# Performance work log

Hardware: AMD Instinct MI355X
Metric: run time of the kernel (lower is better)

The kernel has to match this reference:

```python
import jax, jax.numpy as jnp
import numpy as np

T, B, V, E, H = 256, 64, 10000, 400, 1152


def _n(k, shape, scale=0.05):
    return jax.random.normal(k, shape, jnp.float32) * scale


def setup_inputs() -> dict:
    key = jax.random.key(0)
    ks = jax.random.split(key, 32)
    inp = {}
    inp["x"] = jax.random.randint(ks[0], (T, B), 0, V)
    inp["h0"] = _n(ks[1], (B, H)); inp["h1"] = _n(ks[2], (B, H)); inp["h2"] = _n(ks[3], (B, E))
    inp["c0"] = _n(ks[4], (B, H)); inp["c1"] = _n(ks[5], (B, H)); inp["c2"] = _n(ks[6], (B, E))
    inp["emb"] = _n(ks[7], (V, E), 0.1)
    # layer i: (input_dim, output_dim): (E,H), (H,H), (H,E)
    sizes = [(E, H), (H, H), (H, E)]
    j = 8
    for i, (din, dout) in enumerate(sizes):
        inp[f"W_ih{i}"] = _n(ks[j], (4 * dout, din)); j += 1
        inp[f"W_hh{i}"] = _n(ks[j], (4 * dout, dout)); j += 1
        inp[f"b_ih{i}"] = _n(ks[j], (4 * dout,)); j += 1
        inp[f"b_hh{i}"] = _n(ks[j], (4 * dout,)); j += 1
    inp["dec_W"] = _n(ks[j], (V, E)); j += 1
    inp["dec_b"] = jnp.zeros((V,), jnp.float32)
    return inp


def lstm_cell(x, h, c, Wih, Whh, bih, bhh):
    # PyTorch LSTMCell: gates = x@Wih^T + bih + h@Whh^T + bhh, order i,f,g,o
    g = x @ Wih.T + h @ Whh.T + bih + bhh
    i, f, gg, o = jnp.split(g, 4, axis=-1)
    c2 = jax.nn.sigmoid(f) * c + jax.nn.sigmoid(i) * jnp.tanh(gg)
    h2 = jax.nn.sigmoid(o) * jnp.tanh(c2)
    return h2, c2


def reference(x, h0, h1, h2, c0, c1, c2, emb,
              W_ih0, W_hh0, b_ih0, b_hh0,
              W_ih1, W_hh1, b_ih1, b_hh1,
              W_ih2, W_hh2, b_ih2, b_hh2,
              dec_W, dec_b):
    xe = emb[x]  # [T, B, E]

    def step(carry, xt):
        a0, a1, a2, s0, s1, s2 = carry
        a0, s0 = lstm_cell(xt, a0, s0, W_ih0, W_hh0, b_ih0, b_hh0)
        a1, s1 = lstm_cell(a0, a1, s1, W_ih1, W_hh1, b_ih1, b_hh1)
        a2, s2 = lstm_cell(a1, a2, s2, W_ih2, W_hh2, b_ih2, b_hh2)
        return (a0, a1, a2, s0, s1, s2), a2

    _, out = jax.lax.scan(step, (h0, h1, h2, c0, c1, c2), xe)  # out: [T, B, E]
    decoded = out @ dec_W.T + dec_b  # [T, B, V]
    return decoded
```

## Files before the change

kernel.cpp:

```cpp
#include <hip/hip_runtime.h>
#include <hip/hip_bf16.h>

typedef __hip_bfloat16 bf16;
typedef __attribute__((ext_vector_type(8))) short short8;
typedef __attribute__((ext_vector_type(4))) float f32x4;

#define T_ 256
#define B_ 64
#define V_ 10000
#define E_ 400
#define H_ 1152
#define KU 2304
#define XW 416
#define KD 416
#define XET (XW*B_)
#define NBLK 169

#define MFMA16 __builtin_amdgcn_mfma_f32_16x16x32_bf16
#define ATL(p) __hip_atomic_load((p), __ATOMIC_RELAXED, __HIP_MEMORY_SCOPE_AGENT)
#define ATS(p, v) __hip_atomic_store((p), (v), __ATOMIC_RELAXED, __HIP_MEMORY_SCOPE_AGENT)
#define PIN(x) asm volatile("" : "+v"(x))


__global__ __launch_bounds__(256) void prep_wint(
    const float* __restrict__ s1, int w1,
    const float* __restrict__ s2, int off2, int w2, int Hl,
    bf16* __restrict__ dst, long total)
{
    long i = (long)blockIdx.x * 256 + threadIdx.x;
    if (i >= total) return;
    int r = (int)(i / KU), k = (int)(i % KU);
    int hcol = r >> 2, gate = r & 3;
    long srow = (long)gate * Hl + hcol;
    float v = 0.f;
    if (k < w1) v = s1[srow * w1 + k];
    else if (k >= off2 && k < off2 + w2) v = s2[srow * w2 + (k - off2)];
    dst[i] = __float2bfloat16(v);
}

__global__ __launch_bounds__(256) void prep_wcat(
    const float* __restrict__ s1, int w1,
    bf16* __restrict__ dst, int Ktot, long total)
{
    long i = (long)blockIdx.x * 256 + threadIdx.x;
    if (i >= total) return;
    int k = (int)(i % Ktot);
    long n = i / Ktot;
    dst[i] = __float2bfloat16(k < w1 ? s1[n * w1 + k] : 0.f);
}

__global__ __launch_bounds__(256) void bias_int(
    const float* __restrict__ a, const float* __restrict__ b,
    int Hl, float* __restrict__ d, int n)
{
    int r = blockIdx.x * 256 + threadIdx.x;
    if (r >= n) return;
    int hcol = r >> 2, gate = r & 3;
    d[r] = a[gate * Hl + hcol] + b[gate * Hl + hcol];
}

__global__ __launch_bounds__(256) void gather_xef(
    const int* __restrict__ x, const float* __restrict__ emb,
    bf16* __restrict__ XEf)
{
    long i = (long)blockIdx.x * 256 + threadIdx.x;
    if (i >= (long)T_ * B_ * XW) return;
    int k = (int)(i % XW);
    int b = (int)((i / XW) % B_);
    int t = (int)(i / ((long)XW * B_));
    float v = (k < E_) ? emb[(long)x[t * B_ + b] * E_ + k] : 0.f;
    XEf[(long)t * XET + (((k >> 3) * 64 + b) << 3) + (k & 7)] = __float2bfloat16(v);
}

__global__ __launch_bounds__(256) void copy_hf(
    const float* __restrict__ src, bf16* __restrict__ dst, int cols, int total)
{
    int i = blockIdx.x * 256 + threadIdx.x;
    if (i >= total) return;
    int k = i % cols, b = i / cols;
    dst[(((k >> 3) * 64 + b) << 3) + (k & 7)] = __float2bfloat16(src[(long)b * cols + k]);
}

__global__ __launch_bounds__(256) void copy_f32(
    const float* __restrict__ src, float* __restrict__ dst, int n)
{
    int i = blockIdx.x * 256 + threadIdx.x;
    if (i < n) dst[i] = src[i];
}

__device__ __forceinline__ void grid_bar(int* flags, int* gen, int phase) {
    asm volatile("s_waitcnt vmcnt(0)" ::: "memory");
    __syncthreads();
    if (blockIdx.x == 0) {
        if (threadIdx.x < 64) {
            const int ln = threadIdx.x;
            if (ln == 0) ATS(&flags[0], phase);
            for (;;) {
                int f0 = (ln       < NBLK) ? ATL(&flags[ln])       : phase;
                int f1 = (ln + 64  < NBLK) ? ATL(&flags[ln + 64])  : phase;
                int f2 = (ln + 128 < NBLK) ? ATL(&flags[ln + 128]) : phase;
                if (__all(f0 >= phase && f1 >= phase && f2 >= phase)) break;
                __builtin_amdgcn_s_sleep(1);
            }
            if (ln == 0) {
                ATS(gen, phase);
                __builtin_amdgcn_fence(__ATOMIC_ACQUIRE, "agent");
            }
        }
    } else {
        if (threadIdx.x == 0) {
            ATS(&flags[blockIdx.x], phase);
            while (ATL(gen) < phase)
                __builtin_amdgcn_s_sleep(1);
            __builtin_amdgcn_fence(__ATOMIC_ACQUIRE, "agent");
        }
    }
    __syncthreads();
    asm volatile("" ::: "memory");
}

struct Frag4 { short8 f0, f1, f2, f3; };

__global__ __launch_bounds__(512, 2) void awd_persistent(
    const bf16* __restrict__ XEf,
    const bf16* __restrict__ W0, const bf16* __restrict__ W1, const bf16* __restrict__ W2,
    const float* __restrict__ b0, const float* __restrict__ b1, const float* __restrict__ b2,
    bf16* H0f0, bf16* H0f1, bf16* H1f0, bf16* H1f1, bf16* H2f0, bf16* H2f1,
    float* c0, float* c1, float* c2, bf16* OUTB,
    int* flags, int* gen)
{
    __shared__ float gsm[4][64][65];
    const int bid = blockIdx.x;
    const int tid = threadIdx.x;
    const int lane = tid & 63;
    const int w8 = tid >> 6;
    const int lh = lane >> 4, l15 = lane & 15;
    const int boff8 = (lh * 64 + l15) * 8;

    int layer, grp;
    if (bid < 72)       { layer = 1; grp = bid; }
    else if (bid < 144) { layer = 0; grp = bid - 72; }
    else                { layer = 2; grp = bid - 144; }

    const bf16* Wp  = (layer == 0) ? W0 : (layer == 1) ? W1 : W2;
    const float* bias = (layer == 0) ? b0 : (layer == 1) ? b1 : b2;
    const float* cbuf = (layer == 0) ? c0 : (layer == 1) ? c1 : c2;
    const int Hl  = (layer == 2) ? 400 : 1152;
    const int bkt = (layer == 0) ? 13 : 36;
    const int nkt = (layer == 1) ? 72 : 49;
    const int KT  = (layer == 1) ? 9  : 7;
    const int kbase = w8 * KT;

    short8 wreg[9][4];
    #pragma unroll
    for (int u = 0; u < 9; ++u)
        if (u < KT) {
            #pragma unroll
            for (int rt = 0; rt < 4; ++rt) {
                int row = grp * 64 + rt * 16 + l15;
                int k   = (kbase + u) * 32 + lh * 8;
                wreg[u][rt] = *(const short8*)(Wp + (long)row * KU + k);
                PIN(wreg[u][rt]);
            }
        }

    float myb[2][4];
    #pragma unroll
    for (int e = 0; e < 2; ++e)
        #pragma unroll
        for (int g = 0; g < 4; ++g)
            myb[e][g] = bias[grp * 64 + (w8 + e * 8) * 4 + g];

    float creg[2];
    #pragma unroll
    for (int e = 0; e < 2; ++e)
        creg[e] = cbuf[(long)lane * Hl + grp * 16 + w8 + e * 8];

    for (int s = -1; s <= 256; ++s) {
        bool active = (layer == 0) ? (s <= 254)
                    : (layer == 1) ? (s >= 0 && s <= 255)
                                   : (s >= 1);
        if (active) {
            const int p = s & 1, q = p ^ 1;
            const bf16 *A1, *A2; bf16* hfW; bf16* ob = nullptr;
            if (layer == 0) {
                A1 = XEf + (long)(s + 1) * XET;
                A2 = p ? H0f1 : H0f0;
                hfW = q ? H0f1 : H0f0;
            } else if (layer == 1) {
                A1 = p ? H0f1 : H0f0;
                A2 = q ? H1f1 : H1f0;
                hfW = p ? H1f1 : H1f0;
            } else {
                A1 = q ? H1f1 : H1f0;
                A2 = p ? H2f1 : H2f0;
                hfW = q ? H2f1 : H2f0;
                ob = OUTB + (long)(s - 1) * B_ * XW;
            }

            auto loadf = [&](int u) -> Frag4 {
                const int ktg = kbase + u;
                const bf16* src; int ktL;
                if (ktg < bkt)      { src = A1; ktL = ktg; }
                else if (ktg < nkt) { src = A2; ktL = ktg - bkt; }
                else                { src = A1; ktL = 0; }
                const bf16* pB = src + ktL * 2048 + boff8;
                Frag4 r;
                r.f0 = *(const short8*)(pB);
                r.f1 = *(const short8*)(pB + 128);
                r.f2 = *(const short8*)(pB + 256);
                r.f3 = *(const short8*)(pB + 384);
                return r;
            };

            f32x4 acc[4][4];
            #pragma unroll
            for (int rt = 0; rt < 4; ++rt)
                #pragma unroll
                for (int m = 0; m < 4; ++m)
                    acc[rt][m] = (f32x4){0.f, 0.f, 0.f, 0.f};

            auto domfma = [&](int u, const Frag4& f) {
                #pragma unroll
                for (int rt = 0; rt < 4; ++rt) {
                    acc[rt][0] = MFMA16(wreg[u][rt], f.f0, acc[rt][0], 0, 0, 0);
                    acc[rt][1] = MFMA16(wreg[u][rt], f.f1, acc[rt][1], 0, 0, 0);
                    acc[rt][2] = MFMA16(wreg[u][rt], f.f2, acc[rt][2], 0, 0, 0);
                    acc[rt][3] = MFMA16(wreg[u][rt], f.f3, acc[rt][3], 0, 0, 0);
                }
            };

            #pragma unroll
            for (int u = 0; u < 9; ++u)
                if (u < KT) {
                    Frag4 f = loadf(u);
                    domfma(u, f);
                }

            __syncthreads();
            if (w8 >= 4) {
                #pragma unroll
                for (int rt = 0; rt < 4; ++rt)
                    #pragma unroll
                    for (int m = 0; m < 4; ++m)
                        #pragma unroll
                        for (int r = 0; r < 4; ++r)
                            gsm[w8 - 4][rt * 16 + lh * 4 + r][m * 16 + l15] = acc[rt][m][r];
            }
            __syncthreads();
            if (w8 < 4) {
                #pragma unroll
                for (int rt = 0; rt < 4; ++rt)
                    #pragma unroll
                    for (int m = 0; m < 4; ++m)
                        #pragma unroll
                        for (int r = 0; r < 4; ++r)
                            gsm[w8][rt * 16 + lh * 4 + r][m * 16 + l15] += acc[rt][m][r];
            }
            __syncthreads();

            #pragma unroll
            for (int e = 0; e < 2; ++e) {
                int b = lane;
                int cl = w8 + e * 8;
                float gv[4];
                #pragma unroll
                for (int g = 0; g < 4; ++g)
                    gv[g] = gsm[0][cl * 4 + g][b] + gsm[1][cl * 4 + g][b]
                          + gsm[2][cl * 4 + g][b] + gsm[3][cl * 4 + g][b] + myb[e][g];
                int colG = grp * 16 + cl;
                float c_old = creg[e];
                float i_s = 1.f / (1.f + expf(-gv[0]));
                float f_s = 1.f / (1.f + expf(-gv[1]));
                float o_s = 1.f / (1.f + expf(-gv[3]));
                float c_new = f_s * c_old + i_s * tanhf(gv[2]);
                float hval = o_s * tanhf(c_new);
                creg[e] = c_new;
                bf16 hb = __float2bfloat16(hval);
                unsigned short hbits;
                __builtin_memcpy(&hbits, &hb, 2);
                ATS((unsigned short*)&hfW[(((colG >> 3) * 64 + b) << 3) + (colG & 7)], hbits);
                if (layer == 2) ob[(long)b * XW + colG] = hb;
            }
        }
        grid_bar(flags, gen, s + 2);
    }
}

__global__ __launch_bounds__(256) void decoder(
    const bf16* __restrict__ A, const bf16* __restrict__ W,
    const float* __restrict__ bias, float* __restrict__ out)
{
    const int tid = threadIdx.x;
    const int lane = tid & 63;
    const int w = tid >> 6;
    const int n0 = blockIdx.x * 64;
    const int m0 = blockIdx.y * 64 + w * 16;
    const int c16 = lane & 15;
    const int kg = lane >> 4;

    f32x4 acc[4];
    for (int i = 0; i < 4; ++i) acc[i] = (f32x4){0.f, 0.f, 0.f, 0.f};

    const bf16* arow = A + (long)(m0 + c16) * KD + kg * 8;
    #pragma unroll
    for (int kt = 0; kt < 13; ++kt) {
        short8 af = *(const short8*)(arow + kt * 32);
        #pragma unroll
        for (int ns = 0; ns < 4; ++ns) {
            int n = n0 + ns * 16 + c16;
            if (n > V_ - 1) n = V_ - 1;
            short8 bfr = *(const short8*)(W + (long)n * KD + kt * 32 + kg * 8);
            acc[ns] = MFMA16(af, bfr, acc[ns], 0, 0, 0);
        }
    }

    #pragma unroll
    for (int ns = 0; ns < 4; ++ns) {
        int col = n0 + ns * 16 + c16;
        if (col < V_) {
            float bv = bias[col];
            #pragma unroll
            for (int r = 0; r < 4; ++r) {
                int row = m0 + kg * 4 + r;
                out[(size_t)row * V_ + col] = acc[ns][r] + bv;
            }
        }
    }
}


extern "C" void kernel_launch(void* const* d_in, const int* in_sizes, int n_in,
                              void* d_out, int out_size, void* d_ws, size_t ws_size,
                              hipStream_t stream)
{
    const int*   x    = (const int*)d_in[0];
    const float* h0   = (const float*)d_in[1];
    const float* h1   = (const float*)d_in[2];
    const float* h2   = (const float*)d_in[3];
    const float* c0   = (const float*)d_in[4];
    const float* c1   = (const float*)d_in[5];
    const float* c2   = (const float*)d_in[6];
    const float* emb  = (const float*)d_in[7];
    const float* Wih0 = (const float*)d_in[8];
    const float* Whh0 = (const float*)d_in[9];
    const float* bih0 = (const float*)d_in[10];
    const float* bhh0 = (const float*)d_in[11];
    const float* Wih1 = (const float*)d_in[12];
    const float* Whh1 = (const float*)d_in[13];
    const float* bih1 = (const float*)d_in[14];
    const float* bhh1 = (const float*)d_in[15];
    const float* Wih2 = (const float*)d_in[16];
    const float* Whh2 = (const float*)d_in[17];
    const float* bih2 = (const float*)d_in[18];
    const float* bhh2 = (const float*)d_in[19];
    const float* decW = (const float*)d_in[20];
    const float* decb = (const float*)d_in[21];

    char* wsb = (char*)d_ws;
    size_t off = 0;
    auto alloc = [&](size_t bytes) -> void* {
        void* ptr = wsb + off;
        off = (off + bytes + 255) & ~(size_t)255;
        return ptr;
    };

    bf16* W0i = (bf16*)alloc((size_t)4608 * KU * 2);
    bf16* W1i = (bf16*)alloc((size_t)4608 * KU * 2);
    bf16* W2i = (bf16*)alloc((size_t)1600 * KU * 2);
    bf16* Wdc = (bf16*)alloc((size_t)V_ * KD * 2);
    float* b0i = (float*)alloc(4608 * 4);
    float* b1i = (float*)alloc(4608 * 4);
    float* b2i = (float*)alloc(1600 * 4);
    bf16* XEf = (bf16*)alloc((size_t)T_ * XET * 2);
    bf16* H0f0 = (bf16*)alloc((size_t)B_ * H_ * 2);
    bf16* H0f1 = (bf16*)alloc((size_t)B_ * H_ * 2);
    bf16* H1f0 = (bf16*)alloc((size_t)B_ * H_ * 2);
    bf16* H1f1 = (bf16*)alloc((size_t)B_ * H_ * 2);
    bf16* H2f0 = (bf16*)alloc((size_t)B_ * XW * 2);
    bf16* H2f1 = (bf16*)alloc((size_t)B_ * XW * 2);
    float* c0b = (float*)alloc((size_t)B_ * H_ * 4);
    float* c1b = (float*)alloc((size_t)B_ * H_ * 4);
    float* c2b = (float*)alloc((size_t)B_ * E_ * 4);
    bf16* OUTB = (bf16*)alloc((size_t)T_ * B_ * XW * 2);
    int* gbar = (int*)alloc(2048);

    auto cdiv = [](long a, long b) { return (int)((a + b - 1) / b); };

    hipMemsetAsync(gbar, 0, 2048, stream);

    prep_wint<<<cdiv(4608L * KU, 256), 256, 0, stream>>>(Wih0, 400,  Whh0, 416,  1152, 1152, W0i, 4608L * KU);
    prep_wint<<<cdiv(4608L * KU, 256), 256, 0, stream>>>(Wih1, 1152, Whh1, 1152, 1152, 1152, W1i, 4608L * KU);
    prep_wint<<<cdiv(1600L * KU, 256), 256, 0, stream>>>(Wih2, 1152, Whh2, 1152, 400,  400,  W2i, 1600L * KU);
    prep_wcat<<<cdiv((long)V_ * KD, 256), 256, 0, stream>>>(decW, 400, Wdc, KD, (long)V_ * KD);
    bias_int<<<cdiv(4608, 256), 256, 0, stream>>>(bih0, bhh0, 1152, b0i, 4608);
    bias_int<<<cdiv(4608, 256), 256, 0, stream>>>(bih1, bhh1, 1152, b1i, 4608);
    bias_int<<<cdiv(1600, 256), 256, 0, stream>>>(bih2, bhh2, 400,  b2i, 1600);
    gather_xef<<<cdiv((long)T_ * B_ * XW, 256), 256, 0, stream>>>(x, emb, XEf);

    hipMemsetAsync(H2f0, 0, (size_t)B_ * XW * 2, stream);
    hipMemsetAsync(H2f1, 0, (size_t)B_ * XW * 2, stream);
    hipMemsetAsync(OUTB, 0, (size_t)T_ * B_ * XW * 2, stream);

    copy_hf<<<cdiv(B_ * H_, 256), 256, 0, stream>>>(h0, H0f1, H_, B_ * H_);
    copy_hf<<<cdiv(B_ * H_, 256), 256, 0, stream>>>(h1, H1f1, H_, B_ * H_);
    copy_hf<<<cdiv(B_ * E_, 256), 256, 0, stream>>>(h2, H2f1, E_, B_ * E_);
    copy_f32<<<cdiv(B_ * H_, 256), 256, 0, stream>>>(c0, c0b, B_ * H_);
    copy_f32<<<cdiv(B_ * H_, 256), 256, 0, stream>>>(c1, c1b, B_ * H_);
    copy_f32<<<cdiv(B_ * E_, 256), 256, 0, stream>>>(c2, c2b, B_ * E_);

    {
        int* flags = gbar;
        int* gen   = gbar + 448;
        void* args[] = {
            (void*)&XEf, (void*)&W0i, (void*)&W1i, (void*)&W2i,
            (void*)&b0i, (void*)&b1i, (void*)&b2i,
            (void*)&H0f0, (void*)&H0f1, (void*)&H1f0, (void*)&H1f1,
            (void*)&H2f0, (void*)&H2f1,
            (void*)&c0b, (void*)&c1b, (void*)&c2b, (void*)&OUTB,
            (void*)&flags, (void*)&gen
        };
        hipLaunchCooperativeKernel((void*)awd_persistent, dim3(NBLK), dim3(512),
                                   args, 0, stream);
    }

    decoder<<<dim3((V_ + 63) / 64, (T_ * B_) / 64), 256, 0, stream>>>(
        OUTB, Wdc, decb, (float*)d_out);
}
```

Baseline: 3.644 ms.

## Decentralize grid barrier, single-pass gate reduction, vectorized hidden-state stores

The grid barrier drops the block-0 coordinator and generation flag: every block publishes its flag and one wavefront polls all block flags directly, removing a serial hop per step. The cross-wave gate reduction writes all 8 waves' partial sums into a doubled shared buffer in one pass, cutting two block syncs. New h values are staged in shared memory and written out as 64-bit atomic stores and 16-byte vector stores instead of scattered 2-byte stores. The cost is more shared memory per block (which may affect 2-blocks-per-CU occupancy) and many more blocks polling the same global flags each step.

```diff
diff --git a/kernel.cpp b/kernel.cpp
--- a/kernel.cpp
+++ b/kernel.cpp
@@ -88,32 +88,21 @@
     if (i < n) dst[i] = src[i];
 }
 
-__device__ __forceinline__ void grid_bar(int* flags, int* gen, int phase) {
+__device__ __forceinline__ void grid_bar(int* flags, int phase) {
     asm volatile("s_waitcnt vmcnt(0)" ::: "memory");
     __syncthreads();
-    if (blockIdx.x == 0) {
-        if (threadIdx.x < 64) {
-            const int ln = threadIdx.x;
-            if (ln == 0) ATS(&flags[0], phase);
-            for (;;) {
-                int f0 = (ln       < NBLK) ? ATL(&flags[ln])       : phase;
-                int f1 = (ln + 64  < NBLK) ? ATL(&flags[ln + 64])  : phase;
-                int f2 = (ln + 128 < NBLK) ? ATL(&flags[ln + 128]) : phase;
-                if (__all(f0 >= phase && f1 >= phase && f2 >= phase)) break;
-                __builtin_amdgcn_s_sleep(1);
-            }
-            if (ln == 0) {
-                ATS(gen, phase);
-                __builtin_amdgcn_fence(__ATOMIC_ACQUIRE, "agent");
-            }
+    if (threadIdx.x < 64) {
+        const int ln = threadIdx.x;
+        if (ln == 0) ATS(&flags[blockIdx.x], phase);
+        for (;;) {
+            int f0 = (ln       < NBLK) ? ATL(&flags[ln])       : phase;
+            int f1 = (ln + 64  < NBLK) ? ATL(&flags[ln + 64])  : phase;
+            int f2 = (ln + 128 < NBLK) ? ATL(&flags[ln + 128]) : phase;
+            if (__all(f0 >= phase && f1 >= phase && f2 >= phase)) break;
+            __builtin_amdgcn_s_sleep(1);
         }
-    } else {
-        if (threadIdx.x == 0) {
-            ATS(&flags[blockIdx.x], phase);
-            while (ATL(gen) < phase)
-                __builtin_amdgcn_s_sleep(1);
+        if (ln == 0)
             __builtin_amdgcn_fence(__ATOMIC_ACQUIRE, "agent");
-        }
     }
     __syncthreads();
     asm volatile("" ::: "memory");
@@ -127,9 +116,10 @@
     const float* __restrict__ b0, const float* __restrict__ b1, const float* __restrict__ b2,
     bf16* H0f0, bf16* H0f1, bf16* H1f0, bf16* H1f1, bf16* H2f0, bf16* H2f1,
     float* c0, float* c1, float* c2, bf16* OUTB,
-    int* flags, int* gen)
-{
-    __shared__ float gsm[4][64][65];
+    int* flags)
+{
+    __shared__ float gsm[2][4][64][65];
+    __shared__ unsigned short hsm[64][24];
     const int bid = blockIdx.x;
     const int tid = threadIdx.x;
     const int lane = tid & 63;
@@ -237,26 +227,13 @@
                     domfma(u, f);
                 }
 
-            __syncthreads();
-            if (w8 >= 4) {
+            #pragma unroll
+            for (int rt = 0; rt < 4; ++rt)
                 #pragma unroll
-                for (int rt = 0; rt < 4; ++rt)
+                for (int m = 0; m < 4; ++m)
                     #pragma unroll
-                    for (int m = 0; m < 4; ++m)
-                        #pragma unroll
-                        for (int r = 0; r < 4; ++r)
-                            gsm[w8 - 4][rt * 16 + lh * 4 + r][m * 16 + l15] = acc[rt][m][r];
-            }
-            __syncthreads();
-            if (w8 < 4) {
-                #pragma unroll
-                for (int rt = 0; rt < 4; ++rt)
-                    #pragma unroll
-                    for (int m = 0; m < 4; ++m)
-                        #pragma unroll
-                        for (int r = 0; r < 4; ++r)
-                            gsm[w8][rt * 16 + lh * 4 + r][m * 16 + l15] += acc[rt][m][r];
-            }
+                    for (int r = 0; r < 4; ++r)
+                        gsm[w8 >> 2][w8 & 3][rt * 16 + lh * 4 + r][m * 16 + l15] = acc[rt][m][r];
             __syncthreads();
 
             #pragma unroll
@@ -265,10 +242,13 @@
                 int cl = w8 + e * 8;
                 float gv[4];
                 #pragma unroll
-                for (int g = 0; g < 4; ++g)
-                    gv[g] = gsm[0][cl * 4 + g][b] + gsm[1][cl * 4 + g][b]
-                          + gsm[2][cl * 4 + g][b] + gsm[3][cl * 4 + g][b] + myb[e][g];
-                int colG = grp * 16 + cl;
+                for (int g = 0; g < 4; ++g) {
+                    float v = myb[e][g];
+                    #pragma unroll
+                    for (int kq = 0; kq < 4; ++kq)
+                        v += gsm[0][kq][cl * 4 + g][b] + gsm[1][kq][cl * 4 + g][b];
+                    gv[g] = v;
+                }
                 float c_old = creg[e];
                 float i_s = 1.f / (1.f + expf(-gv[0]));
                 float f_s = 1.f / (1.f + expf(-gv[1]));
@@ -279,11 +259,26 @@
                 bf16 hb = __float2bfloat16(hval);
                 unsigned short hbits;
                 __builtin_memcpy(&hbits, &hb, 2);
-                ATS((unsigned short*)&hfW[(((colG >> 3) * 64 + b) << 3) + (colG & 7)], hbits);
-                if (layer == 2) ob[(long)b * XW + colG] = hb;
+                hsm[b][cl] = hbits;
+            }
+            __syncthreads();
+
+            if (w8 < 2) {
+                unsigned long long v0, v1;
+                __builtin_memcpy(&v0, &hsm[lane][w8 * 8], 8);
+                __builtin_memcpy(&v1, &hsm[lane][w8 * 8 + 4], 8);
+                unsigned long long* qp =
+                    (unsigned long long*)(hfW + (((long)grp * 2 + w8) * 64 + lane) * 8);
+                ATS(qp, v0);
+                ATS(qp + 1, v1);
+            } else if (w8 == 2 && layer == 2) {
+                short8 v0 = *(const short8*)&hsm[lane][0];
+                short8 v1 = *(const short8*)&hsm[lane][8];
+                *(short8*)(ob + (long)lane * XW + grp * 16) = v0;
+                *(short8*)(ob + (long)lane * XW + grp * 16 + 8) = v1;
             }
         }
-        grid_bar(flags, gen, s + 2);
+        grid_bar(flags, s + 2);
     }
 }
 
@@ -411,14 +406,13 @@
 
     {
         int* flags = gbar;
-        int* gen   = gbar + 448;
         void* args[] = {
             (void*)&XEf, (void*)&W0i, (void*)&W1i, (void*)&W2i,
             (void*)&b0i, (void*)&b1i, (void*)&b2i,
             (void*)&H0f0, (void*)&H0f1, (void*)&H1f0, (void*)&H1f1,
             (void*)&H2f0, (void*)&H2f1,
             (void*)&c0b, (void*)&c1b, (void*)&c2b, (void*)&OUTB,
-            (void*)&flags, (void*)&gen
+            (void*)&flags
         };
         hipLaunchCooperativeKernel((void*)awd_persistent, dim3(NBLK), dim3(512),
                                    args, 0, stream);
```

New measurement: 3.944 ms. +8.3%, slower.
